# Kernel tuning notes

Hardware: AMD Instinct MI355X
Metric: run time of the kernel (lower is better)

Reference implementation:

```python
import jax, jax.numpy as jnp
import numpy as np

B, S, D = 2, 2048, 1024
H, DK, DV = 16, 64, 64


def setup_inputs() -> dict:
    key = jax.random.key(0)
    ks = jax.random.split(key, 9)
    s = 0.02
    return {
        "x": jax.random.normal(ks[0], (B, S, D), dtype=jnp.float32),
        "mask": jnp.zeros((B, S), dtype=bool),  # True = padded position
        "Wq": jax.random.normal(ks[1], (D, H * DK), dtype=jnp.float32) * s,
        "bq": jnp.zeros((H * DK,), dtype=jnp.float32),
        "Wk": jax.random.normal(ks[2], (D, H * DK), dtype=jnp.float32) * s,
        "bk": jnp.zeros((H * DK,), dtype=jnp.float32),
        "Wv": jax.random.normal(ks[3], (D, H * DV), dtype=jnp.float32) * s,
        "bv": jnp.zeros((H * DV,), dtype=jnp.float32),
        "Wo": jax.random.normal(ks[4], (H * DV, D), dtype=jnp.float32) * s,
        "bo": jnp.zeros((D,), dtype=jnp.float32),
    }


def reference(x, mask, Wq, bq, Wk, bk, Wv, bv, Wo, bo):
    Bx, Sx, _ = x.shape
    # projections -> [B, H, S, dk/dv]
    q = (x @ Wq + bq).reshape(Bx, Sx, H, DK).transpose(0, 2, 1, 3)
    k = (x @ Wk + bk).reshape(Bx, Sx, H, DK).transpose(0, 2, 1, 3)
    v = (x @ Wv + bv).reshape(Bx, Sx, H, DV).transpose(0, 2, 1, 3)
    # scaled QK^T: [B, H, Sq, Sk]
    scores = jnp.einsum("bhqd,bhkd->bhqk", q, k) / jnp.sqrt(jnp.float32(DK))
    neg_inf = jnp.float32(-jnp.inf)
    # padding mask: True masks out key positions
    scores = jnp.where(mask[:, None, None, :], neg_inf, scores)
    # causal mask
    causal = jnp.triu(jnp.ones((Sx, Sx), dtype=bool), k=1)
    scores = jnp.where(causal[None, None, :, :], neg_inf, scores)
    attn = jax.nn.softmax(scores, axis=-1)
    out = jnp.einsum("bhqk,bhkd->bhqd", attn, v)  # [B, H, S, dv]
    out = out.transpose(0, 2, 1, 3).reshape(Bx, Sx, H * DV)
    return out @ Wo + bo
```

## Files before the change

kernel.cpp:

```cpp
#include <hip/hip_runtime.h>
#include <stdint.h>

typedef __bf16 bf16_t;
typedef __bf16 bf16x8 __attribute__((ext_vector_type(8)));
typedef float f32x4 __attribute__((ext_vector_type(4)));

#define S_LEN 2048
#define D_MODEL 1024
#define NH 16
#define DKV 64
#define BATCH 2

#define QSCALE 0.1803368801111204f

__device__ __forceinline__ uint16_t f2bfu(float f) {
    union { float f; uint32_t u; } c; c.f = f;
    return (uint16_t)((c.u + 0x7fffu + ((c.u >> 16) & 1u)) >> 16);
}
__device__ __forceinline__ bf16_t f2bf(float f) {
    union { uint16_t s; bf16_t b; } o; o.s = f2bfu(f);
    return o.b;
}
__device__ __forceinline__ uint32_t pack2t(float lo, float hi) {
    union { float f; uint32_t u; } a, b; a.f = lo; b.f = hi;
    return (a.u >> 16) | (b.u & 0xFFFF0000u);
}
__device__ __forceinline__ void gld_lds16(const bf16_t* g, bf16_t* l) {
    __builtin_amdgcn_global_load_lds(
        (const __attribute__((address_space(1))) void*)g,
        (__attribute__((address_space(3))) void*)l, 16, 0, 0);
}

__global__ __launch_bounds__(256) void k_convert_x(const float* __restrict__ x,
                                                   bf16_t* __restrict__ xb, int n) {
    int i = (blockIdx.x * 256 + threadIdx.x) * 4;
    if (i < n) {
        float4 v = *(const float4*)(x + i);
        xb[i + 0] = f2bf(v.x);
        xb[i + 1] = f2bf(v.y);
        xb[i + 2] = f2bf(v.z);
        xb[i + 3] = f2bf(v.w);
    }
}

__global__ __launch_bounds__(256) void k_transpose4(
    const float* __restrict__ Wq, const float* __restrict__ Wk,
    const float* __restrict__ Wv, const float* __restrict__ Wo,
    bf16_t* __restrict__ WqkvT, bf16_t* __restrict__ WoT) {
    __shared__ float tile[64][65];
    int k0 = blockIdx.x * 64;
    int n0 = blockIdx.y * 64;
    const float* W; bf16_t* WT; int np, nw;
    if (n0 < 3072) {
        W = (n0 < 1024) ? Wq : (n0 < 2048) ? Wk : Wv;
        np = n0 & 1023; WT = WqkvT; nw = n0;
    } else {
        W = Wo; np = n0 - 3072; WT = WoT; nw = n0 - 3072;
    }
    int tx = threadIdx.x & 63, ty = threadIdx.x >> 6;
    #pragma unroll
    for (int r = ty; r < 64; r += 4)
        tile[r][tx] = W[(size_t)(k0 + r) * 1024 + np + tx];
    __syncthreads();
    #pragma unroll
    for (int r = ty; r < 64; r += 4)
        WT[(size_t)(nw + r) * 1024 + k0 + tx] = f2bf(tile[tx][r]);
}

#define BM 128
#define BN 128
#define BKK 64

template <int MODE>
__global__ __launch_bounds__(256) void k_gemm_bt(
    const bf16_t* __restrict__ A, const bf16_t* __restrict__ BT,
    int M, int N, int K,
    const float* __restrict__ bias0, const float* __restrict__ bias1,
    const float* __restrict__ bias2,
    float* __restrict__ outF,
    bf16_t* __restrict__ outQ, bf16_t* __restrict__ outK, bf16_t* __restrict__ outVt) {
    __shared__ __align__(16) bf16_t As[BM * BKK];
    __shared__ __align__(16) bf16_t Bs[BN * BKK];
    int m0 = blockIdx.x * BM;
    int n0 = blockIdx.y * BN;
    int t = threadIdx.x;
    int wid = t >> 6, lane = t & 63, l15 = lane & 15, quad = lane >> 4;
    int wr = (wid >> 1) * 64, wc = (wid & 1) * 64;
    int srow = t >> 3;
    int schunk = (t & 7) ^ (srow & 7);
    int sldst = (t & 7) * 8;
    const f32x4 fzero = {0.f, 0.f, 0.f, 0.f};
    f32x4 acc[4][4];
    #pragma unroll
    for (int i = 0; i < 4; i++)
        #pragma unroll
        for (int j = 0; j < 4; j++) acc[i][j] = fzero;

    int r7 = l15 & 7;
    for (int k0 = 0; k0 < K; k0 += BKK) {
        #pragma unroll
        for (int p = 0; p < 4; p++) {
            int r = p * 32 + srow;
            gld_lds16(&A[(size_t)(m0 + r) * K + k0 + schunk * 8], &As[r * 64 + sldst]);
            gld_lds16(&BT[(size_t)(n0 + r) * K + k0 + schunk * 8], &Bs[r * 64 + sldst]);
        }
        __syncthreads();
        #pragma unroll
        for (int kk = 0; kk < BKK; kk += 32) {
            int g = quad + (kk >> 3);
            int col = ((g ^ r7) << 3);
            bf16x8 af[4], bfr[4];
            #pragma unroll
            for (int mt = 0; mt < 4; mt++)
                af[mt] = *(const bf16x8*)&As[(wr + mt * 16 + l15) * 64 + col];
            #pragma unroll
            for (int nt = 0; nt < 4; nt++)
                bfr[nt] = *(const bf16x8*)&Bs[(wc + nt * 16 + l15) * 64 + col];
            #pragma unroll
            for (int mt = 0; mt < 4; mt++)
                #pragma unroll
                for (int nt = 0; nt < 4; nt++)
                    acc[mt][nt] = __builtin_amdgcn_mfma_f32_16x16x32_bf16(
                        af[mt], bfr[nt], acc[mt][nt], 0, 0, 0);
        }
        __syncthreads();
    }

    #pragma unroll
    for (int mt = 0; mt < 4; mt++) {
        #pragma unroll
        for (int nt = 0; nt < 4; nt++) {
            if (MODE == 0) {
                int gc = n0 + wc + nt * 16 + l15;
                int sec = gc >> 10;
                int nn = gc & 1023;
                int h = nn >> 6, d = nn & 63;
                int gr0 = m0 + wr + mt * 16 + quad * 4;
                int b = gr0 >> 11, s0 = gr0 & 2047;
                if (sec == 2) {
                    float bv = bias2[nn];
                    uint32_t lo = (uint32_t)f2bfu(acc[mt][nt][0] + bv) |
                                  ((uint32_t)f2bfu(acc[mt][nt][1] + bv) << 16);
                    uint32_t hi = (uint32_t)f2bfu(acc[mt][nt][2] + bv) |
                                  ((uint32_t)f2bfu(acc[mt][nt][3] + bv) << 16);
                    uint2 pk; pk.x = lo; pk.y = hi;
                    *(uint2*)&outVt[(((size_t)(b * NH + h)) * DKV + d) * S_LEN + s0] = pk;
                } else {
                    const float* bias = (sec == 0) ? bias0 : bias1;
                    float bv = bias[nn];
                    #pragma unroll
                    for (int r = 0; r < 4; r++) {
                        float val = acc[mt][nt][r] + bv;
                        size_t idx = (((size_t)(b * NH + h)) * S_LEN + s0 + r) * DKV + d;
                        if (sec == 0) outQ[idx] = f2bf(val * QSCALE);
                        else          outK[idx] = f2bf(val);
                    }
                }
            } else {
                #pragma unroll
                for (int r = 0; r < 4; r++) {
                    int gr = m0 + wr + mt * 16 + quad * 4 + r;
                    int gc = n0 + wc + nt * 16 + l15;
                    outF[(size_t)gr * N + gc] = acc[mt][nt][r] + bias0[gc];
                }
            }
        }
    }
}

#define APD 72

__global__ __launch_bounds__(256) void k_attn7(
    const bf16_t* __restrict__ Q, const bf16_t* __restrict__ Kg,
    const bf16_t* __restrict__ Vt, const unsigned char* __restrict__ mask,
    bf16_t* __restrict__ O) {
    __shared__ __align__(16) char qps_raw[64 * APD * sizeof(bf16_t)];
    bf16_t (*Qs)[APD] = (bf16_t(*)[APD])qps_raw;
    bf16_t (*Ps)[16][APD] = (bf16_t(*)[16][APD])qps_raw;
    __shared__ __align__(16) bf16_t Ks[64 * 64];
    __shared__ __align__(16) bf16_t Vs[64 * 64];
    __shared__ float maskS[64];

    int bid = blockIdx.x;
    int bh = bid & 31;
    int u = bid >> 5;
    int a = u & 7, g2 = u >> 3;
    int qt = (g2 == 0) ? 31 - a : (g2 == 1) ? a : (g2 == 2) ? 23 - a : 8 + a;
    int b = bh >> 4, h = bh & 15;
    int t = threadIdx.x;
    int w = t >> 6, lane = t & 63, l15 = lane & 15, quad = lane >> 4;

    const bf16_t* Qbase = Q + ((size_t)bh * S_LEN + qt * 64) * DKV;
    {
        int r = t >> 3, c = (t & 7) * 8;
        *(uint4*)&Qs[r][c]      = *(const uint4*)&Qbase[(size_t)r * 64 + c];
        *(uint4*)&Qs[r + 32][c] = *(const uint4*)&Qbase[(size_t)(r + 32) * 64 + c];
    }
    __syncthreads();
    bf16x8 qf0 = *(const bf16x8*)&Qs[w * 16 + l15][quad * 8];
    bf16x8 qf1 = *(const bf16x8*)&Qs[w * 16 + l15][32 + quad * 8];

    const f32x4 fzero = {0.f, 0.f, 0.f, 0.f};
    f32x4 oacc[4];
    f32x4 lacc = fzero;
    #pragma unroll
    for (int nt = 0; nt < 4; nt++) oacc[nt] = fzero;

    const bf16_t one_b = (bf16_t)1.0f;
    const bf16x8 onesf = {one_b, one_b, one_b, one_b, one_b, one_b, one_b, one_b};

    int qg   = qt * 64 + w * 16 + l15;
    int qmin = qt * 64 + w * 16;
    int r7 = l15 & 7;

    int sr = t >> 3;
    int sc = (t & 7) ^ (sr & 7);
    int sl = (t & 7) * 8;

    for (int kt = 0; kt <= qt; kt++) {
        __syncthreads();
        {
            const bf16_t* Kb = Kg + ((size_t)bh * S_LEN + kt * 64) * DKV;
            #pragma unroll
            for (int p = 0; p < 2; p++) {
                int r = p * 32 + sr;
                gld_lds16(&Kb[(size_t)r * 64 + sc * 8], &Ks[r * 64 + sl]);
                gld_lds16(&Vt[((size_t)bh * DKV + r) * S_LEN + kt * 64 + sc * 8],
                          &Vs[r * 64 + sl]);
            }
        }
        if (t < 64) maskS[t] = mask[b * S_LEN + kt * 64 + t] ? -1e30f : 0.0f;
        __syncthreads();

        int kbase = kt * 64;

        f32x4 sacc[4];
        #pragma unroll
        for (int mt = 0; mt < 4; mt++) sacc[mt] = fzero;
        #pragma unroll
        for (int kk = 0; kk < 64; kk += 32) {
            bf16x8 qf = kk ? qf1 : qf0;
            int g = quad + (kk >> 3);
            int col = ((g ^ r7) << 3);
            #pragma unroll
            for (int mt = 0; mt < 4; mt++) {
                bf16x8 af = *(const bf16x8*)&Ks[(mt * 16 + l15) * 64 + col];
                sacc[mt] = __builtin_amdgcn_mfma_f32_16x16x32_bf16(af, qf, sacc[mt], 0, 0, 0);
            }
        }

        bool diag = (kbase + 63 > qmin);
        #pragma unroll
        for (int mt = 0; mt < 4; mt++) {
            float4 m4 = *(const float4*)&maskS[mt * 16 + quad * 4];
            #pragma unroll
            for (int r = 0; r < 4; r++)
                sacc[mt][r] += ((const float*)&m4)[r];
            if (diag) {
                int kgb = kbase + mt * 16 + quad * 4;
                #pragma unroll
                for (int r = 0; r < 4; r++)
                    if (kgb + r > qg) sacc[mt][r] = -1e30f;
            }
        }
        #pragma unroll
        for (int mt = 0; mt < 4; mt++) {
            uint32_t p0 = pack2t(exp2f(sacc[mt][0]), exp2f(sacc[mt][1]));
            uint32_t p1 = pack2t(exp2f(sacc[mt][2]), exp2f(sacc[mt][3]));
            union { uint32_t u[2]; uint2 v; } pk; pk.u[0] = p0; pk.u[1] = p1;
            *(uint2*)&Ps[w][l15][mt * 16 + quad * 4] = pk.v;
        }

        #pragma unroll
        for (int kk = 0; kk < 64; kk += 32) {
            bf16x8 pf = *(const bf16x8*)&Ps[w][l15][kk + quad * 8];
            int g = quad + (kk >> 3);
            int vcol = ((g ^ r7) << 3);
            #pragma unroll
            for (int nt = 0; nt < 4; nt++) {
                bf16x8 vf = *(const bf16x8*)&Vs[(nt * 16 + l15) * 64 + vcol];
                oacc[nt] = __builtin_amdgcn_mfma_f32_16x16x32_bf16(pf, vf, oacc[nt], 0, 0, 0);
            }
            lacc = __builtin_amdgcn_mfma_f32_16x16x32_bf16(pf, onesf, lacc, 0, 0, 0);
        }
    }

    #pragma unroll
    for (int r = 0; r < 4; r++) {
        float l = lacc[r];
        float invl = l > 0.f ? 1.f / l : 0.f;
        int q = qt * 64 + w * 16 + quad * 4 + r;
        #pragma unroll
        for (int nt = 0; nt < 4; nt++) {
            int d = nt * 16 + l15;
            O[((size_t)b * S_LEN + q) * D_MODEL + h * DKV + d] = f2bf(oacc[nt][r] * invl);
        }
    }
}

extern "C" void kernel_launch(void* const* d_in, const int* in_sizes, int n_in,
                              void* d_out, int out_size, void* d_ws, size_t ws_size,
                              hipStream_t stream) {
    const float* x = (const float*)d_in[0];
    const unsigned char* mask = (const unsigned char*)d_in[1];
    const float* Wq = (const float*)d_in[2];
    const float* bq = (const float*)d_in[3];
    const float* Wk = (const float*)d_in[4];
    const float* bk = (const float*)d_in[5];
    const float* Wv = (const float*)d_in[6];
    const float* bv = (const float*)d_in[7];
    const float* Wo = (const float*)d_in[8];
    const float* bo = (const float*)d_in[9];
    float* out = (float*)d_out;

    char* ws = (char*)d_ws;
    const size_t MB = 1024 * 1024;
    bf16_t* xb    = (bf16_t*)(ws + 0 * MB);
    bf16_t* WqkvT = (bf16_t*)(ws + 8 * MB);
    bf16_t* WoT   = (bf16_t*)(ws + 14 * MB);
    bf16_t* Qb    = (bf16_t*)(ws + 16 * MB);
    bf16_t* Kb    = (bf16_t*)(ws + 24 * MB);
    bf16_t* Vtb   = (bf16_t*)(ws + 32 * MB);
    bf16_t* AOb   = (bf16_t*)(ws + 40 * MB);

    k_convert_x<<<dim3(4096), dim3(256), 0, stream>>>(x, xb, 4 * 1024 * 1024);
    k_transpose4<<<dim3(16, 64), dim3(256), 0, stream>>>(Wq, Wk, Wv, Wo, WqkvT, WoT);
    k_gemm_bt<0><<<dim3(32, 24), dim3(256), 0, stream>>>(
        xb, WqkvT, 4096, 3072, 1024, bq, bk, bv, nullptr, Qb, Kb, Vtb);
    k_attn7<<<dim3(1024), dim3(256), 0, stream>>>(Qb, Kb, Vtb, mask, AOb);
    k_gemm_bt<1><<<dim3(32, 8), dim3(256), 0, stream>>>(
        AOb, WoT, 4096, 1024, 1024, bo, nullptr, nullptr, out,
        nullptr, nullptr, nullptr);
}
```

Before: 201.9 us.

## Use 128-key attention tiles and a dedicated 128x64 output-projection GEMM

The attention kernel now loads 128 keys and values per iteration and processes them as two 64-key sub-tiles. This halves the number of barrier-separated load phases and breaks early on the causal diagonal. Block scheduling is simplified to a plain descending qt order in place of the interleaved mapping. The output projection gets its own 128x64-tile kernel, which doubles the grid to 512 blocks for better CU occupancy. The trade-off is larger LDS per attention block (lower occupancy), and the descending order may balance load less evenly than the old interleave.

```diff
diff --git a/kernel.cpp b/kernel.cpp
--- a/kernel.cpp
+++ b/kernel.cpp
@@ -71,13 +71,10 @@
 #define BN 128
 #define BKK 64
 
-template <int MODE>
-__global__ __launch_bounds__(256) void k_gemm_bt(
-    const bf16_t* __restrict__ A, const bf16_t* __restrict__ BT,
-    int M, int N, int K,
+__global__ __launch_bounds__(256) void k_gemm_qkv(
+    const bf16_t* __restrict__ A, const bf16_t* __restrict__ BT, int K,
     const float* __restrict__ bias0, const float* __restrict__ bias1,
     const float* __restrict__ bias2,
-    float* __restrict__ outF,
     bf16_t* __restrict__ outQ, bf16_t* __restrict__ outK, bf16_t* __restrict__ outVt) {
     __shared__ __align__(16) bf16_t As[BM * BKK];
     __shared__ __align__(16) bf16_t Bs[BN * BKK];
@@ -130,39 +127,98 @@
     for (int mt = 0; mt < 4; mt++) {
         #pragma unroll
         for (int nt = 0; nt < 4; nt++) {
-            if (MODE == 0) {
-                int gc = n0 + wc + nt * 16 + l15;
-                int sec = gc >> 10;
-                int nn = gc & 1023;
-                int h = nn >> 6, d = nn & 63;
-                int gr0 = m0 + wr + mt * 16 + quad * 4;
-                int b = gr0 >> 11, s0 = gr0 & 2047;
-                if (sec == 2) {
-                    float bv = bias2[nn];
-                    uint32_t lo = (uint32_t)f2bfu(acc[mt][nt][0] + bv) |
-                                  ((uint32_t)f2bfu(acc[mt][nt][1] + bv) << 16);
-                    uint32_t hi = (uint32_t)f2bfu(acc[mt][nt][2] + bv) |
-                                  ((uint32_t)f2bfu(acc[mt][nt][3] + bv) << 16);
-                    uint2 pk; pk.x = lo; pk.y = hi;
-                    *(uint2*)&outVt[(((size_t)(b * NH + h)) * DKV + d) * S_LEN + s0] = pk;
-                } else {
-                    const float* bias = (sec == 0) ? bias0 : bias1;
-                    float bv = bias[nn];
-                    #pragma unroll
-                    for (int r = 0; r < 4; r++) {
-                        float val = acc[mt][nt][r] + bv;
-                        size_t idx = (((size_t)(b * NH + h)) * S_LEN + s0 + r) * DKV + d;
-                        if (sec == 0) outQ[idx] = f2bf(val * QSCALE);
-                        else          outK[idx] = f2bf(val);
-                    }
+            int gc = n0 + wc + nt * 16 + l15;
+            int sec = gc >> 10;
+            int nn = gc & 1023;
+            int h = nn >> 6, d = nn & 63;
+            int gr0 = m0 + wr + mt * 16 + quad * 4;
+            int b = gr0 >> 11, s0 = gr0 & 2047;
+            if (sec == 2) {
+                float bv = bias2[nn];
+                uint32_t lo = (uint32_t)f2bfu(acc[mt][nt][0] + bv) |
+                              ((uint32_t)f2bfu(acc[mt][nt][1] + bv) << 16);
+                uint32_t hi = (uint32_t)f2bfu(acc[mt][nt][2] + bv) |
+                              ((uint32_t)f2bfu(acc[mt][nt][3] + bv) << 16);
+                uint2 pk; pk.x = lo; pk.y = hi;
+                *(uint2*)&outVt[(((size_t)(b * NH + h)) * DKV + d) * S_LEN + s0] = pk;
+            } else {
+                const float* bias = (sec == 0) ? bias0 : bias1;
+                float bv = bias[nn];
+                #pragma unroll
+                for (int r = 0; r < 4; r++) {
+                    float val = acc[mt][nt][r] + bv;
+                    size_t idx = (((size_t)(b * NH + h)) * S_LEN + s0 + r) * DKV + d;
+                    if (sec == 0) outQ[idx] = f2bf(val * QSCALE);
+                    else          outK[idx] = f2bf(val);
                 }
-            } else {
-                #pragma unroll
-                for (int r = 0; r < 4; r++) {
-                    int gr = m0 + wr + mt * 16 + quad * 4 + r;
-                    int gc = n0 + wc + nt * 16 + l15;
-                    outF[(size_t)gr * N + gc] = acc[mt][nt][r] + bias0[gc];
-                }
+            }
+        }
+    }
+}
+
+__global__ __launch_bounds__(256) void k_gemm_out(
+    const bf16_t* __restrict__ A, const bf16_t* __restrict__ BT, int N, int K,
+    const float* __restrict__ bias, float* __restrict__ outF) {
+    __shared__ __align__(16) bf16_t As[128 * 64];
+    __shared__ __align__(16) bf16_t Bs[64 * 64];
+    int m0 = blockIdx.x * 128;
+    int n0 = blockIdx.y * 64;
+    int t = threadIdx.x;
+    int wid = t >> 6, lane = t & 63, l15 = lane & 15, quad = lane >> 4;
+    int wr = wid * 32;
+    int srow = t >> 3;
+    int schunk = (t & 7) ^ (srow & 7);
+    int sldst = (t & 7) * 8;
+    const f32x4 fzero = {0.f, 0.f, 0.f, 0.f};
+    f32x4 acc[2][4];
+    #pragma unroll
+    for (int i = 0; i < 2; i++)
+        #pragma unroll
+        for (int j = 0; j < 4; j++) acc[i][j] = fzero;
+
+    int r7 = l15 & 7;
+    for (int k0 = 0; k0 < K; k0 += 64) {
+        #pragma unroll
+        for (int p = 0; p < 4; p++) {
+            int r = p * 32 + srow;
+            gld_lds16(&A[(size_t)(m0 + r) * K + k0 + schunk * 8], &As[r * 64 + sldst]);
+        }
+        #pragma unroll
+        for (int p = 0; p < 2; p++) {
+            int r = p * 32 + srow;
+            gld_lds16(&BT[(size_t)(n0 + r) * K + k0 + schunk * 8], &Bs[r * 64 + sldst]);
+        }
+        __syncthreads();
+        #pragma unroll
+        for (int kk = 0; kk < 64; kk += 32) {
+            int g = quad + (kk >> 3);
+            int col = ((g ^ r7) << 3);
+            bf16x8 af[2], bfr[4];
+            #pragma unroll
+            for (int mt = 0; mt < 2; mt++)
+                af[mt] = *(const bf16x8*)&As[(wr + mt * 16 + l15) * 64 + col];
+            #pragma unroll
+            for (int nt = 0; nt < 4; nt++)
+                bfr[nt] = *(const bf16x8*)&Bs[(nt * 16 + l15) * 64 + col];
+            #pragma unroll
+            for (int mt = 0; mt < 2; mt++)
+                #pragma unroll
+                for (int nt = 0; nt < 4; nt++)
+                    acc[mt][nt] = __builtin_amdgcn_mfma_f32_16x16x32_bf16(
+                        af[mt], bfr[nt], acc[mt][nt], 0, 0, 0);
+        }
+        __syncthreads();
+    }
+
+    #pragma unroll
+    for (int mt = 0; mt < 2; mt++) {
+        #pragma unroll
+        for (int nt = 0; nt < 4; nt++) {
+            #pragma unroll
+            for (int r = 0; r < 4; r++) {
+                int gr = m0 + wr + mt * 16 + quad * 4 + r;
+                int gc = n0 + nt * 16 + l15;
+                outF[(size_t)gr * N + gc] = acc[mt][nt][r] + bias[gc];
             }
         }
     }
@@ -170,22 +226,20 @@
 
 #define APD 72
 
-__global__ __launch_bounds__(256) void k_attn7(
+__global__ __launch_bounds__(256) void k_attn6(
     const bf16_t* __restrict__ Q, const bf16_t* __restrict__ Kg,
     const bf16_t* __restrict__ Vt, const unsigned char* __restrict__ mask,
     bf16_t* __restrict__ O) {
     __shared__ __align__(16) char qps_raw[64 * APD * sizeof(bf16_t)];
     bf16_t (*Qs)[APD] = (bf16_t(*)[APD])qps_raw;
     bf16_t (*Ps)[16][APD] = (bf16_t(*)[16][APD])qps_raw;
-    __shared__ __align__(16) bf16_t Ks[64 * 64];
-    __shared__ __align__(16) bf16_t Vs[64 * 64];
-    __shared__ float maskS[64];
+    __shared__ __align__(16) bf16_t Ks[128 * 64];
+    __shared__ __align__(16) bf16_t Vs[64 * 128];
+    __shared__ float maskS[128];
 
     int bid = blockIdx.x;
     int bh = bid & 31;
-    int u = bid >> 5;
-    int a = u & 7, g2 = u >> 3;
-    int qt = (g2 == 0) ? 31 - a : (g2 == 1) ? a : (g2 == 2) ? 23 - a : 8 + a;
+    int qt = 31 - (bid >> 5);
     int b = bh >> 4, h = bh & 15;
     int t = threadIdx.x;
     int w = t >> 6, lane = t & 63, l15 = lane & 15, quad = lane >> 4;
@@ -211,77 +265,90 @@
 
     int qg   = qt * 64 + w * 16 + l15;
     int qmin = qt * 64 + w * 16;
+    int qmax = qmin + 15;
+    int ktmax = qt >> 1;
     int r7 = l15 & 7;
 
-    int sr = t >> 3;
-    int sc = (t & 7) ^ (sr & 7);
-    int sl = (t & 7) * 8;
-
-    for (int kt = 0; kt <= qt; kt++) {
+    int srK = t >> 3;
+    int scK = (t & 7) ^ (srK & 7);
+    int slK = (t & 7) * 8;
+    int srV = t >> 4;
+    int scV = (t & 15) ^ (srV & 7);
+    int slV = (t & 15) * 8;
+
+    for (int kt = 0; kt <= ktmax; kt++) {
         __syncthreads();
         {
-            const bf16_t* Kb = Kg + ((size_t)bh * S_LEN + kt * 64) * DKV;
-            #pragma unroll
-            for (int p = 0; p < 2; p++) {
-                int r = p * 32 + sr;
-                gld_lds16(&Kb[(size_t)r * 64 + sc * 8], &Ks[r * 64 + sl]);
-                gld_lds16(&Vt[((size_t)bh * DKV + r) * S_LEN + kt * 64 + sc * 8],
-                          &Vs[r * 64 + sl]);
-            }
-        }
-        if (t < 64) maskS[t] = mask[b * S_LEN + kt * 64 + t] ? -1e30f : 0.0f;
-        __syncthreads();
-
-        int kbase = kt * 64;
-
-        f32x4 sacc[4];
-        #pragma unroll
-        for (int mt = 0; mt < 4; mt++) sacc[mt] = fzero;
-        #pragma unroll
-        for (int kk = 0; kk < 64; kk += 32) {
-            bf16x8 qf = kk ? qf1 : qf0;
-            int g = quad + (kk >> 3);
-            int col = ((g ^ r7) << 3);
+            const bf16_t* Kb = Kg + ((size_t)bh * S_LEN + kt * 128) * DKV;
+            #pragma unroll
+            for (int p = 0; p < 4; p++) {
+                int r = p * 32 + srK;
+                gld_lds16(&Kb[(size_t)r * 64 + scK * 8], &Ks[r * 64 + slK]);
+            }
+            #pragma unroll
+            for (int p = 0; p < 4; p++) {
+                int r = p * 16 + srV;
+                gld_lds16(&Vt[((size_t)bh * DKV + r) * S_LEN + kt * 128 + scV * 8],
+                          &Vs[r * 128 + slV]);
+            }
+        }
+        if (t < 128) maskS[t] = mask[b * S_LEN + kt * 128 + t] ? -1e30f : 0.0f;
+        __syncthreads();
+
+        #pragma unroll
+        for (int sub = 0; sub < 2; sub++) {
+            int kbase = kt * 128 + sub * 64;
+            if (kbase > qmax) break;
+
+            f32x4 sacc[4];
+            #pragma unroll
+            for (int mt = 0; mt < 4; mt++) sacc[mt] = fzero;
+            #pragma unroll
+            for (int kk = 0; kk < 64; kk += 32) {
+                bf16x8 qf = kk ? qf1 : qf0;
+                int g = quad + (kk >> 3);
+                int col = ((g ^ r7) << 3);
+                #pragma unroll
+                for (int mt = 0; mt < 4; mt++) {
+                    bf16x8 af = *(const bf16x8*)&Ks[(sub * 64 + mt * 16 + l15) * 64 + col];
+                    sacc[mt] = __builtin_amdgcn_mfma_f32_16x16x32_bf16(af, qf, sacc[mt], 0, 0, 0);
+                }
+            }
+
+            bool diag = (kbase + 63 > qmin);
             #pragma unroll
             for (int mt = 0; mt < 4; mt++) {
-                bf16x8 af = *(const bf16x8*)&Ks[(mt * 16 + l15) * 64 + col];
-                sacc[mt] = __builtin_amdgcn_mfma_f32_16x16x32_bf16(af, qf, sacc[mt], 0, 0, 0);
-            }
-        }
-
-        bool diag = (kbase + 63 > qmin);
-        #pragma unroll
-        for (int mt = 0; mt < 4; mt++) {
-            float4 m4 = *(const float4*)&maskS[mt * 16 + quad * 4];
-            #pragma unroll
-            for (int r = 0; r < 4; r++)
-                sacc[mt][r] += ((const float*)&m4)[r];
-            if (diag) {
-                int kgb = kbase + mt * 16 + quad * 4;
+                float4 m4 = *(const float4*)&maskS[sub * 64 + mt * 16 + quad * 4];
                 #pragma unroll
                 for (int r = 0; r < 4; r++)
-                    if (kgb + r > qg) sacc[mt][r] = -1e30f;
-            }
-        }
-        #pragma unroll
-        for (int mt = 0; mt < 4; mt++) {
-            uint32_t p0 = pack2t(exp2f(sacc[mt][0]), exp2f(sacc[mt][1]));
-            uint32_t p1 = pack2t(exp2f(sacc[mt][2]), exp2f(sacc[mt][3]));
-            union { uint32_t u[2]; uint2 v; } pk; pk.u[0] = p0; pk.u[1] = p1;
-            *(uint2*)&Ps[w][l15][mt * 16 + quad * 4] = pk.v;
-        }
-
-        #pragma unroll
-        for (int kk = 0; kk < 64; kk += 32) {
-            bf16x8 pf = *(const bf16x8*)&Ps[w][l15][kk + quad * 8];
-            int g = quad + (kk >> 3);
-            int vcol = ((g ^ r7) << 3);
-            #pragma unroll
-            for (int nt = 0; nt < 4; nt++) {
-                bf16x8 vf = *(const bf16x8*)&Vs[(nt * 16 + l15) * 64 + vcol];
-                oacc[nt] = __builtin_amdgcn_mfma_f32_16x16x32_bf16(pf, vf, oacc[nt], 0, 0, 0);
-            }
-            lacc = __builtin_amdgcn_mfma_f32_16x16x32_bf16(pf, onesf, lacc, 0, 0, 0);
+                    sacc[mt][r] += ((const float*)&m4)[r];
+                if (diag) {
+                    int kgb = kbase + mt * 16 + quad * 4;
+                    #pragma unroll
+                    for (int r = 0; r < 4; r++)
+                        if (kgb + r > qg) sacc[mt][r] = -1e30f;
+                }
+            }
+            #pragma unroll
+            for (int mt = 0; mt < 4; mt++) {
+                uint32_t p0 = pack2t(exp2f(sacc[mt][0]), exp2f(sacc[mt][1]));
+                uint32_t p1 = pack2t(exp2f(sacc[mt][2]), exp2f(sacc[mt][3]));
+                union { uint32_t u[2]; uint2 v; } pk; pk.u[0] = p0; pk.u[1] = p1;
+                *(uint2*)&Ps[w][l15][mt * 16 + quad * 4] = pk.v;
+            }
+
+            #pragma unroll
+            for (int kk = 0; kk < 64; kk += 32) {
+                bf16x8 pf = *(const bf16x8*)&Ps[w][l15][kk + quad * 8];
+                int g2 = sub * 8 + (kk >> 3) + quad;
+                int vcol = ((g2 ^ r7) << 3);
+                #pragma unroll
+                for (int nt = 0; nt < 4; nt++) {
+                    bf16x8 vf = *(const bf16x8*)&Vs[(nt * 16 + l15) * 128 + vcol];
+                    oacc[nt] = __builtin_amdgcn_mfma_f32_16x16x32_bf16(pf, vf, oacc[nt], 0, 0, 0);
+                }
+                lacc = __builtin_amdgcn_mfma_f32_16x16x32_bf16(pf, onesf, lacc, 0, 0, 0);
+            }
         }
     }
 
@@ -325,10 +392,9 @@
 
     k_convert_x<<<dim3(4096), dim3(256), 0, stream>>>(x, xb, 4 * 1024 * 1024);
     k_transpose4<<<dim3(16, 64), dim3(256), 0, stream>>>(Wq, Wk, Wv, Wo, WqkvT, WoT);
-    k_gemm_bt<0><<<dim3(32, 24), dim3(256), 0, stream>>>(
-        xb, WqkvT, 4096, 3072, 1024, bq, bk, bv, nullptr, Qb, Kb, Vtb);
-    k_attn7<<<dim3(1024), dim3(256), 0, stream>>>(Qb, Kb, Vtb, mask, AOb);
-    k_gemm_bt<1><<<dim3(32, 8), dim3(256), 0, stream>>>(
-        AOb, WoT, 4096, 1024, 1024, bo, nullptr, nullptr, out,
-        nullptr, nullptr, nullptr);
-}
+    k_gemm_qkv<<<dim3(32, 24), dim3(256), 0, stream>>>(
+        xb, WqkvT, 1024, bq, bk, bv, Qb, Kb, Vtb);
+    k_attn6<<<dim3(1024), dim3(256), 0, stream>>>(Qb, Kb, Vtb, mask, AOb);
+    k_gemm_out<<<dim3(32, 16), dim3(256), 0, stream>>>(
+        AOb, WoT, 1024, 1024, bo, out);
+}
```

Result: faster. 191.1 us (-5.3%).
